# Kernel optimization log

Hardware: AMD Instinct MI355X
Metric: run time of the kernel (lower is better)

Reference implementation:

```python
import jax, jax.numpy as jnp
import numpy as np

GROUP = 128          # GPTQ quantization group size
H = 2048             # hidden_size
I = 1408             # moe_intermediate_size
T = 16384            # routed tokens


def _pack_rows(v):
    # v: [in, out] int4 values -> [in//8, out] int32 (8 nibbles per int32 along input dim)
    v = v.reshape(v.shape[0] // 8, 8, v.shape[1]).astype(jnp.int32)
    sh = (4 * jnp.arange(8, dtype=jnp.int32))[None, :, None]
    return (v << sh).sum(axis=1).astype(jnp.int32)


def _pack_cols(v):
    # v: [groups, out] int4 values -> [groups, out//8] int32
    v = v.reshape(v.shape[0], v.shape[1] // 8, 8).astype(jnp.int32)
    sh = (4 * jnp.arange(8, dtype=jnp.int32))[None, None, :]
    return (v << sh).sum(axis=-1).astype(jnp.int32)


def _unpack_rows(qw):
    # [in//8, out] int32 -> [in, out] int4 values
    sh = 4 * jnp.arange(8, dtype=jnp.int32)
    v = (qw[:, None, :] >> sh[None, :, None]) & 0xF
    return v.reshape(qw.shape[0] * 8, qw.shape[1])


def _unpack_cols(qz):
    # [groups, out//8] int32 -> [groups, out] int4 values
    sh = 4 * jnp.arange(8, dtype=jnp.int32)
    v = (qz[:, :, None] >> sh[None, None, :]) & 0xF
    return v.reshape(qz.shape[0], qz.shape[1] * 8)


def _dequant(qw, qz, sc):
    # GPTQ dequant: W[k, n] = (q[k, n] - (zero[g(k), n] + 1)) * scale[g(k), n]
    w = _unpack_rows(qw).astype(sc.dtype)                      # [in, out]
    z = (_unpack_cols(qz) + 1).astype(sc.dtype)                # [groups, out]
    scale = jnp.repeat(sc, GROUP, axis=0)                      # [in, out]
    zero = jnp.repeat(z, GROUP, axis=0)                        # [in, out]
    return (w - zero) * scale


def setup_inputs() -> dict:
    key = jax.random.key(0)
    ks = jax.random.split(key, 10)
    x = jax.random.normal(ks[0], (T, H), dtype=jnp.float32)

    def make_quant(kq, kz, ksc, n_in, n_out):
        q = jax.random.randint(kq, (n_in, n_out), 0, 16, dtype=jnp.int32)
        z = jax.random.randint(kz, (n_in // GROUP, n_out), 0, 15, dtype=jnp.int32)
        sc = jax.random.uniform(ksc, (n_in // GROUP, n_out), dtype=jnp.float32,
                                minval=1e-3, maxval=2e-2)
        return _pack_rows(q), _pack_cols(z), sc

    qw_g, qz_g, sc_g = make_quant(ks[1], ks[2], ks[3], H, I)
    qw_u, qz_u, sc_u = make_quant(ks[4], ks[5], ks[6], H, I)
    qw_d, qz_d, sc_d = make_quant(ks[7], ks[8], ks[9], I, H)
    return {"x": x,
            "qw_gate": qw_g, "qz_gate": qz_g, "sc_gate": sc_g,
            "qw_up": qw_u, "qz_up": qz_u, "sc_up": sc_u,
            "qw_down": qw_d, "qz_down": qz_d, "sc_down": sc_d}


def reference(x, qw_gate, qz_gate, sc_gate, qw_up, qz_up, sc_up,
              qw_down, qz_down, sc_down):
    Wg = _dequant(qw_gate, qz_gate, sc_gate)   # [H, I]
    Wu = _dequant(qw_up, qz_up, sc_up)         # [H, I]
    Wd = _dequant(qw_down, qz_down, sc_down)   # [I, H]
    # fused_gate_up: silu(x @ Wg) * (x @ Wu)
    h = jax.nn.silu(x @ Wg) * (x @ Wu)         # [T, I]
    return h @ Wd                              # [T, H]
```

## Files before the change

### kernel.cpp

```cpp
#include <hip/hip_runtime.h>

#define T_DIM 16384
#define H_DIM 2048
#define I_DIM 1408
#define NB_DIM (2 * I_DIM)

typedef _Float16 half8 __attribute__((ext_vector_type(8)));
typedef float floatx4 __attribute__((ext_vector_type(4)));

__device__ __forceinline__ void async_cp16(const _Float16* gp, _Float16* lp) {
    __builtin_amdgcn_global_load_lds(
        (const __attribute__((address_space(1))) unsigned int*)gp,
        (__attribute__((address_space(3))) unsigned int*)lp,
        16, 0, 0);
}

__global__ void cvt_fp16_kernel(const float* __restrict__ x, _Float16* __restrict__ xh) {
    int i = (blockIdx.x * 256 + threadIdx.x) * 8;
    const float4* p = (const float4*)(x + i);
    float4 a = p[0];
    float4 b = p[1];
    half8 o = { (_Float16)a.x, (_Float16)a.y, (_Float16)a.z, (_Float16)a.w,
                (_Float16)b.x, (_Float16)b.y, (_Float16)b.z, (_Float16)b.w };
    *(half8*)(xh + i) = o;
}

__global__ void dequant_kernel(const int* __restrict__ qw, const int* __restrict__ qz,
                               const float* __restrict__ sc, _Float16* __restrict__ Wt,
                               int K, int N, int interleave, int off) {
    __shared__ half8 tile[256];
    int t = threadIdx.x;
    int nl = t & 63, kl = t >> 6;
    int n  = blockIdx.x * 64 + nl;
    int kp = blockIdx.y * 4 + kl;
    int q = qw[kp * N + n];
    int g = kp >> 4;
    float scale = sc[g * N + n];
    int zq = (qz[g * (N >> 3) + (n >> 3)] >> (4 * (n & 7))) & 0xF;
    float zf = (float)(zq + 1);
    half8 o;
#pragma unroll
    for (int j = 0; j < 8; ++j)
        o[j] = (_Float16)(((float)((q >> (4 * j)) & 0xF) - zf) * scale);
    tile[nl * 4 + kl] = o;
    __syncthreads();
    int nl2 = t >> 2, kl2 = t & 3;
    int n2 = blockIdx.x * 64 + nl2;
    int np = interleave ? (((n2 >> 5) << 6) + (n2 & 31) + off) : n2;
    *(half8*)(Wt + (size_t)np * K + (size_t)(blockIdx.y * 4 + kl2) * 8) = tile[nl2 * 4 + kl2];
}


__launch_bounds__(256, 3)
__global__ void gemm_gateup(const _Float16* __restrict__ A,
                            const _Float16* __restrict__ B,
                            _Float16* __restrict__ h) {
    __shared__ _Float16 As[128 * 64];
    __shared__ _Float16 Bs[128 * 64];
    const int t = threadIdx.x;
    const int wave = t >> 6, lane = t & 63;
    const int m0 = blockIdx.x * 128;
    const int n0 = blockIdx.y * 128;
    const int wm = wave >> 1, wn = wave & 1;

    const int srow = wave * 8 + (lane >> 3);
    const int schunk = (lane & 7) ^ (lane >> 3);
    const _Float16* ag = A + (size_t)(m0 + srow) * H_DIM + schunk * 8;
    const _Float16* bg = B + (size_t)(n0 + srow) * H_DIM + schunk * 8;
    _Float16* lA = As + wave * 512;
    _Float16* lB = Bs + wave * 512;

    const int q4 = lane >> 4, l15 = lane & 15;
    int aoff[4], boff[4];
#pragma unroll
    for (int i = 0; i < 4; ++i) {
        int rA = wm * 64 + i * 16 + l15;
        aoff[i] = rA * 64 + ((q4 ^ (rA & 7)) * 8);
        int rB = wn * 64 + i * 16 + l15;
        boff[i] = rB * 64 + ((q4 ^ (rB & 7)) * 8);
    }

    floatx4 zero = {0.f, 0.f, 0.f, 0.f};
    floatx4 acc[4][4];
#pragma unroll
    for (int mi = 0; mi < 4; ++mi)
#pragma unroll
        for (int ni = 0; ni < 4; ++ni) acc[mi][ni] = zero;

    for (int kt = 0; kt < H_DIM; kt += 64) {
        __syncthreads();
#pragma unroll
        for (int i = 0; i < 4; ++i) {
            async_cp16(ag + kt + (size_t)i * 32 * H_DIM, lA + i * 2048);
            async_cp16(bg + kt + (size_t)i * 32 * H_DIM, lB + i * 2048);
        }
        __syncthreads();
#pragma unroll
        for (int kk = 0; kk < 2; ++kk) {
            half8 af[4], bf[4];
#pragma unroll
            for (int i = 0; i < 4; ++i) af[i] = *(const half8*)(As + (aoff[i] ^ (kk * 32)));
#pragma unroll
            for (int i = 0; i < 4; ++i) bf[i] = *(const half8*)(Bs + (boff[i] ^ (kk * 32)));
#pragma unroll
            for (int mi = 0; mi < 4; ++mi)
#pragma unroll
                for (int ni = 0; ni < 4; ++ni)
                    acc[mi][ni] = __builtin_amdgcn_mfma_f32_16x16x32_f16(af[mi], bf[ni], acc[mi][ni], 0, 0, 0);
        }
    }

    const int rq = q4 * 4;
#pragma unroll
    for (int mi = 0; mi < 4; ++mi)
#pragma unroll
        for (int nc = 0; nc < 2; ++nc)
#pragma unroll
            for (int r = 0; r < 4; ++r) {
                int row = m0 + wm * 64 + mi * 16 + rq + r;
                int col = blockIdx.y * 64 + wn * 32 + nc * 16 + l15;
                float g = acc[mi][nc][r];
                float u = acc[mi][nc + 2][r];
                float s = (g / (1.0f + __expf(-g))) * u;
                h[(size_t)row * I_DIM + col] = (_Float16)s;
            }
}

__launch_bounds__(256, 3)
__global__ void gemm_down(const _Float16* __restrict__ A,
                          const _Float16* __restrict__ B,
                          float* __restrict__ out) {
    __shared__ _Float16 As[128 * 64];
    __shared__ _Float16 Bs[128 * 64];
    const int t = threadIdx.x;
    const int wave = t >> 6, lane = t & 63;
    const int m0 = blockIdx.x * 128;
    const int n0 = blockIdx.y * 128;
    const int wm = wave >> 1, wn = wave & 1;

    const int srow = wave * 8 + (lane >> 3);
    const int schunk = (lane & 7) ^ (lane >> 3);
    const _Float16* ag = A + (size_t)(m0 + srow) * I_DIM + schunk * 8;
    const _Float16* bg = B + (size_t)(n0 + srow) * I_DIM + schunk * 8;
    _Float16* lA = As + wave * 512;
    _Float16* lB = Bs + wave * 512;

    const int q4 = lane >> 4, l15 = lane & 15;
    int aoff[4], boff[4];
#pragma unroll
    for (int i = 0; i < 4; ++i) {
        int rA = wm * 64 + i * 16 + l15;
        aoff[i] = rA * 64 + ((q4 ^ (rA & 7)) * 8);
        int rB = wn * 64 + i * 16 + l15;
        boff[i] = rB * 64 + ((q4 ^ (rB & 7)) * 8);
    }

    floatx4 zero = {0.f, 0.f, 0.f, 0.f};
    floatx4 acc[4][4];
#pragma unroll
    for (int mi = 0; mi < 4; ++mi)
#pragma unroll
        for (int ni = 0; ni < 4; ++ni) acc[mi][ni] = zero;

    for (int kt = 0; kt < I_DIM; kt += 64) {
        __syncthreads();
#pragma unroll
        for (int i = 0; i < 4; ++i) {
            async_cp16(ag + kt + (size_t)i * 32 * I_DIM, lA + i * 2048);
            async_cp16(bg + kt + (size_t)i * 32 * I_DIM, lB + i * 2048);
        }
        __syncthreads();
#pragma unroll
        for (int kk = 0; kk < 2; ++kk) {
            half8 af[4], bf[4];
#pragma unroll
            for (int i = 0; i < 4; ++i) af[i] = *(const half8*)(As + (aoff[i] ^ (kk * 32)));
#pragma unroll
            for (int i = 0; i < 4; ++i) bf[i] = *(const half8*)(Bs + (boff[i] ^ (kk * 32)));
#pragma unroll
            for (int mi = 0; mi < 4; ++mi)
#pragma unroll
                for (int ni = 0; ni < 4; ++ni)
                    acc[mi][ni] = __builtin_amdgcn_mfma_f32_16x16x32_f16(af[mi], bf[ni], acc[mi][ni], 0, 0, 0);
        }
    }

    const int rq = q4 * 4;
#pragma unroll
    for (int mi = 0; mi < 4; ++mi)
#pragma unroll
        for (int ni = 0; ni < 4; ++ni)
#pragma unroll
            for (int r = 0; r < 4; ++r) {
                int row = m0 + wm * 64 + mi * 16 + rq + r;
                int col = n0 + wn * 64 + ni * 16 + l15;
                out[(size_t)row * H_DIM + col] = acc[ni][mi][r];
            }
}


__launch_bounds__(256, 3)
__global__ void gemm_down_fixed(const _Float16* __restrict__ A,
                                const _Float16* __restrict__ B,
                                float* __restrict__ out) {
    __shared__ _Float16 As[128 * 64];
    __shared__ _Float16 Bs[128 * 64];
    const int t = threadIdx.x;
    const int wave = t >> 6, lane = t & 63;
    const int m0 = blockIdx.x * 128;
    const int n0 = blockIdx.y * 128;
    const int wm = wave >> 1, wn = wave & 1;

    const int srow = wave * 8 + (lane >> 3);
    const int schunk = (lane & 7) ^ (lane >> 3);
    const _Float16* ag = A + (size_t)(m0 + srow) * I_DIM + schunk * 8;
    const _Float16* bg = B + (size_t)(n0 + srow) * I_DIM + schunk * 8;
    _Float16* lA = As + wave * 512;
    _Float16* lB = Bs + wave * 512;

    const int q4 = lane >> 4, l15 = lane & 15;
    int aoff[4], boff[4];
#pragma unroll
    for (int i = 0; i < 4; ++i) {
        int rA = wm * 64 + i * 16 + l15;
        aoff[i] = rA * 64 + ((q4 ^ (rA & 7)) * 8);
        int rB = wn * 64 + i * 16 + l15;
        boff[i] = rB * 64 + ((q4 ^ (rB & 7)) * 8);
    }

    floatx4 zero = {0.f, 0.f, 0.f, 0.f};
    floatx4 acc[4][4];
#pragma unroll
    for (int mi = 0; mi < 4; ++mi)
#pragma unroll
        for (int ni = 0; ni < 4; ++ni) acc[mi][ni] = zero;

    for (int kt = 0; kt < I_DIM; kt += 64) {
        __syncthreads();
#pragma unroll
        for (int i = 0; i < 4; ++i) {
            async_cp16(ag + kt + (size_t)i * 32 * I_DIM, lA + i * 2048);
            async_cp16(bg + kt + (size_t)i * 32 * I_DIM, lB + i * 2048);
        }
        __syncthreads();
#pragma unroll
        for (int kk = 0; kk < 2; ++kk) {
            half8 af[4], bf[4];
#pragma unroll
            for (int i = 0; i < 4; ++i) af[i] = *(const half8*)(As + (aoff[i] ^ (kk * 32)));
#pragma unroll
            for (int i = 0; i < 4; ++i) bf[i] = *(const half8*)(Bs + (boff[i] ^ (kk * 32)));
#pragma unroll
            for (int mi = 0; mi < 4; ++mi)
#pragma unroll
                for (int ni = 0; ni < 4; ++ni)
                    acc[mi][ni] = __builtin_amdgcn_mfma_f32_16x16x32_f16(af[mi], bf[ni], acc[mi][ni], 0, 0, 0);
        }
    }

    const int rq = q4 * 4;
#pragma unroll
    for (int mi = 0; mi < 4; ++mi)
#pragma unroll
        for (int ni = 0; ni < 4; ++ni)
#pragma unroll
            for (int r = 0; r < 4; ++r) {
                int row = m0 + wm * 64 + mi * 16 + rq + r;
                int col = n0 + wn * 64 + ni * 16 + l15;
                out[(size_t)row * H_DIM + col] = acc[mi][ni][r];
            }
}

extern "C" void kernel_launch(void* const* d_in, const int* in_sizes, int n_in,
                              void* d_out, int out_size, void* d_ws, size_t ws_size,
                              hipStream_t stream) {
    const float* x    = (const float*)d_in[0];
    const int* qw_g   = (const int*)d_in[1];
    const int* qz_g   = (const int*)d_in[2];
    const float* sc_g = (const float*)d_in[3];
    const int* qw_u   = (const int*)d_in[4];
    const int* qz_u   = (const int*)d_in[5];
    const float* sc_u = (const float*)d_in[6];
    const int* qw_d   = (const int*)d_in[7];
    const int* qz_d   = (const int*)d_in[8];
    const float* sc_d = (const float*)d_in[9];
    float* out = (float*)d_out;

    char* ws = (char*)d_ws;
    _Float16* xh  = (_Float16*)ws;  ws += (size_t)T_DIM * H_DIM * sizeof(_Float16);
    _Float16* hh  = (_Float16*)ws;  ws += (size_t)T_DIM * I_DIM * sizeof(_Float16);
    _Float16* Bgu = (_Float16*)ws;  ws += (size_t)NB_DIM * H_DIM * sizeof(_Float16);
    _Float16* Wd  = (_Float16*)ws;  ws += (size_t)H_DIM * I_DIM * sizeof(_Float16);

    cvt_fp16_kernel<<<(T_DIM * H_DIM) / 2048, 256, 0, stream>>>(x, xh);
    dequant_kernel<<<dim3(I_DIM / 64, H_DIM / 32), 256, 0, stream>>>(qw_g, qz_g, sc_g, Bgu, H_DIM, I_DIM, 1, 0);
    dequant_kernel<<<dim3(I_DIM / 64, H_DIM / 32), 256, 0, stream>>>(qw_u, qz_u, sc_u, Bgu, H_DIM, I_DIM, 1, 32);
    dequant_kernel<<<dim3(H_DIM / 64, I_DIM / 32), 256, 0, stream>>>(qw_d, qz_d, sc_d, Wd, I_DIM, H_DIM, 0, 0);
    gemm_gateup<<<dim3(T_DIM / 128, NB_DIM / 128), 256, 0, stream>>>(xh, Bgu, hh);
    gemm_down_fixed<<<dim3(T_DIM / 128, H_DIM / 128), 256, 0, stream>>>(hh, Wd, out);
}
```

Before: 518.1 us.

## Switch GEMMs to 32x32x16 MFMA tiles and swap grid axis order

Both GEMM kernels replace the 4x4 grid of 16x16x32 MFMAs per wave with a 2x2 grid of 32x32x16 MFMAs. This halves the LDS fragment loads per k-step and uses the larger, denser matrix instruction. The grid is also transposed so consecutive blocks walk the N dimension for one M tile, which improves L2 reuse of activation rows. The epilogue index mapping is rewritten for the 32x32 accumulator layout, and the duplicate down kernel is removed.

```diff
diff --git a/kernel.cpp b/kernel.cpp
--- a/kernel.cpp
+++ b/kernel.cpp
@@ -6,7 +6,7 @@
 #define NB_DIM (2 * I_DIM)
 
 typedef _Float16 half8 __attribute__((ext_vector_type(8)));
-typedef float floatx4 __attribute__((ext_vector_type(4)));
+typedef float floatx16 __attribute__((ext_vector_type(16)));
 
 __device__ __forceinline__ void async_cp16(const _Float16* gp, _Float16* lp) {
     __builtin_amdgcn_global_load_lds(
@@ -59,8 +59,8 @@
     __shared__ _Float16 Bs[128 * 64];
     const int t = threadIdx.x;
     const int wave = t >> 6, lane = t & 63;
-    const int m0 = blockIdx.x * 128;
-    const int n0 = blockIdx.y * 128;
+    const int n0 = blockIdx.x * 128;
+    const int m0 = blockIdx.y * 128;
     const int wm = wave >> 1, wn = wave & 1;
 
     const int srow = wave * 8 + (lane >> 3);
@@ -70,22 +70,23 @@
     _Float16* lA = As + wave * 512;
     _Float16* lB = Bs + wave * 512;
 
-    const int q4 = lane >> 4, l15 = lane & 15;
-    int aoff[4], boff[4];
-#pragma unroll
-    for (int i = 0; i < 4; ++i) {
-        int rA = wm * 64 + i * 16 + l15;
-        aoff[i] = rA * 64 + ((q4 ^ (rA & 7)) * 8);
-        int rB = wn * 64 + i * 16 + l15;
-        boff[i] = rB * 64 + ((q4 ^ (rB & 7)) * 8);
-    }
-
-    floatx4 zero = {0.f, 0.f, 0.f, 0.f};
-    floatx4 acc[4][4];
-#pragma unroll
-    for (int mi = 0; mi < 4; ++mi)
-#pragma unroll
-        for (int ni = 0; ni < 4; ++ni) acc[mi][ni] = zero;
+    const int l31 = lane & 31, h5 = lane >> 5;
+    int arow64[2], arm[2], brow64[2], brm[2];
+#pragma unroll
+    for (int i = 0; i < 2; ++i) {
+        int rA = wm * 64 + i * 32 + l31;
+        arow64[i] = rA * 64; arm[i] = rA & 7;
+        int rB = wn * 64 + i * 32 + l31;
+        brow64[i] = rB * 64; brm[i] = rB & 7;
+    }
+
+    floatx16 acc[2][2];
+#pragma unroll
+    for (int mi = 0; mi < 2; ++mi)
+#pragma unroll
+        for (int ni = 0; ni < 2; ++ni)
+#pragma unroll
+            for (int r = 0; r < 16; ++r) acc[mi][ni][r] = 0.f;
 
     for (int kt = 0; kt < H_DIM; kt += 64) {
         __syncthreads();
@@ -96,34 +97,32 @@
         }
         __syncthreads();
 #pragma unroll
-        for (int kk = 0; kk < 2; ++kk) {
-            half8 af[4], bf[4];
-#pragma unroll
-            for (int i = 0; i < 4; ++i) af[i] = *(const half8*)(As + (aoff[i] ^ (kk * 32)));
-#pragma unroll
-            for (int i = 0; i < 4; ++i) bf[i] = *(const half8*)(Bs + (boff[i] ^ (kk * 32)));
-#pragma unroll
-            for (int mi = 0; mi < 4; ++mi)
-#pragma unroll
-                for (int ni = 0; ni < 4; ++ni)
-                    acc[mi][ni] = __builtin_amdgcn_mfma_f32_16x16x32_f16(af[mi], bf[ni], acc[mi][ni], 0, 0, 0);
-        }
-    }
-
-    const int rq = q4 * 4;
-#pragma unroll
-    for (int mi = 0; mi < 4; ++mi)
-#pragma unroll
-        for (int nc = 0; nc < 2; ++nc)
-#pragma unroll
-            for (int r = 0; r < 4; ++r) {
-                int row = m0 + wm * 64 + mi * 16 + rq + r;
-                int col = blockIdx.y * 64 + wn * 32 + nc * 16 + l15;
-                float g = acc[mi][nc][r];
-                float u = acc[mi][nc + 2][r];
-                float s = (g / (1.0f + __expf(-g))) * u;
-                h[(size_t)row * I_DIM + col] = (_Float16)s;
-            }
+        for (int kk = 0; kk < 4; ++kk) {
+            const int c = h5 + kk * 2;
+            half8 af[2], bf[2];
+#pragma unroll
+            for (int i = 0; i < 2; ++i) af[i] = *(const half8*)(As + arow64[i] + ((c ^ arm[i]) * 8));
+#pragma unroll
+            for (int i = 0; i < 2; ++i) bf[i] = *(const half8*)(Bs + brow64[i] + ((c ^ brm[i]) * 8));
+#pragma unroll
+            for (int mi = 0; mi < 2; ++mi)
+#pragma unroll
+                for (int ni = 0; ni < 2; ++ni)
+                    acc[mi][ni] = __builtin_amdgcn_mfma_f32_32x32x16_f16(af[mi], bf[ni], acc[mi][ni], 0, 0, 0);
+        }
+    }
+
+    const int hcol = (n0 >> 1) + wn * 32 + l31;
+#pragma unroll
+    for (int mi = 0; mi < 2; ++mi)
+#pragma unroll
+        for (int r = 0; r < 16; ++r) {
+            int row = m0 + wm * 64 + mi * 32 + (r & 3) + 8 * (r >> 2) + 4 * h5;
+            float g = acc[mi][0][r];
+            float u = acc[mi][1][r];
+            float s = (g / (1.0f + __expf(-g))) * u;
+            h[(size_t)row * I_DIM + hcol] = (_Float16)s;
+        }
 }
 
 __launch_bounds__(256, 3)
@@ -134,8 +133,8 @@
     __shared__ _Float16 Bs[128 * 64];
     const int t = threadIdx.x;
     const int wave = t >> 6, lane = t & 63;
-    const int m0 = blockIdx.x * 128;
-    const int n0 = blockIdx.y * 128;
+    const int n0 = blockIdx.x * 128;
+    const int m0 = blockIdx.y * 128;
     const int wm = wave >> 1, wn = wave & 1;
 
     const int srow = wave * 8 + (lane >> 3);
@@ -145,22 +144,23 @@
     _Float16* lA = As + wave * 512;
     _Float16* lB = Bs + wave * 512;
 
-    const int q4 = lane >> 4, l15 = lane & 15;
-    int aoff[4], boff[4];
-#pragma unroll
-    for (int i = 0; i < 4; ++i) {
-        int rA = wm * 64 + i * 16 + l15;
-        aoff[i] = rA * 64 + ((q4 ^ (rA & 7)) * 8);
-        int rB = wn * 64 + i * 16 + l15;
-        boff[i] = rB * 64 + ((q4 ^ (rB & 7)) * 8);
-    }
-
-    floatx4 zero = {0.f, 0.f, 0.f, 0.f};
-    floatx4 acc[4][4];
-#pragma unroll
-    for (int mi = 0; mi < 4; ++mi)
-#pragma unroll
-        for (int ni = 0; ni < 4; ++ni) acc[mi][ni] = zero;
+    const int l31 = lane & 31, h5 = lane >> 5;
+    int arow64[2], arm[2], brow64[2], brm[2];
+#pragma unroll
+    for (int i = 0; i < 2; ++i) {
+        int rA = wm * 64 + i * 32 + l31;
+        arow64[i] = rA * 64; arm[i] = rA & 7;
+        int rB = wn * 64 + i * 32 + l31;
+        brow64[i] = rB * 64; brm[i] = rB & 7;
+    }
+
+    floatx16 acc[2][2];
+#pragma unroll
+    for (int mi = 0; mi < 2; ++mi)
+#pragma unroll
+        for (int ni = 0; ni < 2; ++ni)
+#pragma unroll
+            for (int r = 0; r < 16; ++r) acc[mi][ni][r] = 0.f;
 
     for (int kt = 0; kt < I_DIM; kt += 64) {
         __syncthreads();
@@ -171,102 +171,29 @@
         }
         __syncthreads();
 #pragma unroll
-        for (int kk = 0; kk < 2; ++kk) {
-            half8 af[4], bf[4];
-#pragma unroll
-            for (int i = 0; i < 4; ++i) af[i] = *(const half8*)(As + (aoff[i] ^ (kk * 32)));
-#pragma unroll
-            for (int i = 0; i < 4; ++i) bf[i] = *(const half8*)(Bs + (boff[i] ^ (kk * 32)));
-#pragma unroll
-            for (int mi = 0; mi < 4; ++mi)
-#pragma unroll
-                for (int ni = 0; ni < 4; ++ni)
-                    acc[mi][ni] = __builtin_amdgcn_mfma_f32_16x16x32_f16(af[mi], bf[ni], acc[mi][ni], 0, 0, 0);
-        }
-    }
-
-    const int rq = q4 * 4;
-#pragma unroll
-    for (int mi = 0; mi < 4; ++mi)
-#pragma unroll
-        for (int ni = 0; ni < 4; ++ni)
-#pragma unroll
-            for (int r = 0; r < 4; ++r) {
-                int row = m0 + wm * 64 + mi * 16 + rq + r;
-                int col = n0 + wn * 64 + ni * 16 + l15;
-                out[(size_t)row * H_DIM + col] = acc[ni][mi][r];
-            }
-}
-
-
-__launch_bounds__(256, 3)
-__global__ void gemm_down_fixed(const _Float16* __restrict__ A,
-                                const _Float16* __restrict__ B,
-                                float* __restrict__ out) {
-    __shared__ _Float16 As[128 * 64];
-    __shared__ _Float16 Bs[128 * 64];
-    const int t = threadIdx.x;
-    const int wave = t >> 6, lane = t & 63;
-    const int m0 = blockIdx.x * 128;
-    const int n0 = blockIdx.y * 128;
-    const int wm = wave >> 1, wn = wave & 1;
-
-    const int srow = wave * 8 + (lane >> 3);
-    const int schunk = (lane & 7) ^ (lane >> 3);
-    const _Float16* ag = A + (size_t)(m0 + srow) * I_DIM + schunk * 8;
-    const _Float16* bg = B + (size_t)(n0 + srow) * I_DIM + schunk * 8;
-    _Float16* lA = As + wave * 512;
-    _Float16* lB = Bs + wave * 512;
-
-    const int q4 = lane >> 4, l15 = lane & 15;
-    int aoff[4], boff[4];
-#pragma unroll
-    for (int i = 0; i < 4; ++i) {
-        int rA = wm * 64 + i * 16 + l15;
-        aoff[i] = rA * 64 + ((q4 ^ (rA & 7)) * 8);
-        int rB = wn * 64 + i * 16 + l15;
-        boff[i] = rB * 64 + ((q4 ^ (rB & 7)) * 8);
-    }
-
-    floatx4 zero = {0.f, 0.f, 0.f, 0.f};
-    floatx4 acc[4][4];
-#pragma unroll
-    for (int mi = 0; mi < 4; ++mi)
-#pragma unroll
-        for (int ni = 0; ni < 4; ++ni) acc[mi][ni] = zero;
-
-    for (int kt = 0; kt < I_DIM; kt += 64) {
-        __syncthreads();
-#pragma unroll
-        for (int i = 0; i < 4; ++i) {
-            async_cp16(ag + kt + (size_t)i * 32 * I_DIM, lA + i * 2048);
-            async_cp16(bg + kt + (size_t)i * 32 * I_DIM, lB + i * 2048);
-        }
-        __syncthreads();
-#pragma unroll
-        for (int kk = 0; kk < 2; ++kk) {
-            half8 af[4], bf[4];
-#pragma unroll
-            for (int i = 0; i < 4; ++i) af[i] = *(const half8*)(As + (aoff[i] ^ (kk * 32)));
-#pragma unroll
-            for (int i = 0; i < 4; ++i) bf[i] = *(const half8*)(Bs + (boff[i] ^ (kk * 32)));
-#pragma unroll
-            for (int mi = 0; mi < 4; ++mi)
-#pragma unroll
-                for (int ni = 0; ni < 4; ++ni)
-                    acc[mi][ni] = __builtin_amdgcn_mfma_f32_16x16x32_f16(af[mi], bf[ni], acc[mi][ni], 0, 0, 0);
-        }
-    }
-
-    const int rq = q4 * 4;
-#pragma unroll
-    for (int mi = 0; mi < 4; ++mi)
-#pragma unroll
-        for (int ni = 0; ni < 4; ++ni)
-#pragma unroll
-            for (int r = 0; r < 4; ++r) {
-                int row = m0 + wm * 64 + mi * 16 + rq + r;
-                int col = n0 + wn * 64 + ni * 16 + l15;
+        for (int kk = 0; kk < 4; ++kk) {
+            const int c = h5 + kk * 2;
+            half8 af[2], bf[2];
+#pragma unroll
+            for (int i = 0; i < 2; ++i) af[i] = *(const half8*)(As + arow64[i] + ((c ^ arm[i]) * 8));
+#pragma unroll
+            for (int i = 0; i < 2; ++i) bf[i] = *(const half8*)(Bs + brow64[i] + ((c ^ brm[i]) * 8));
+#pragma unroll
+            for (int mi = 0; mi < 2; ++mi)
+#pragma unroll
+                for (int ni = 0; ni < 2; ++ni)
+                    acc[mi][ni] = __builtin_amdgcn_mfma_f32_32x32x16_f16(af[mi], bf[ni], acc[mi][ni], 0, 0, 0);
+        }
+    }
+
+#pragma unroll
+    for (int mi = 0; mi < 2; ++mi)
+#pragma unroll
+        for (int ni = 0; ni < 2; ++ni)
+#pragma unroll
+            for (int r = 0; r < 16; ++r) {
+                int row = m0 + wm * 64 + mi * 32 + (r & 3) + 8 * (r >> 2) + 4 * h5;
+                int col = n0 + wn * 64 + ni * 32 + l31;
                 out[(size_t)row * H_DIM + col] = acc[mi][ni][r];
             }
 }
@@ -290,12 +217,12 @@
     _Float16* xh  = (_Float16*)ws;  ws += (size_t)T_DIM * H_DIM * sizeof(_Float16);
     _Float16* hh  = (_Float16*)ws;  ws += (size_t)T_DIM * I_DIM * sizeof(_Float16);
     _Float16* Bgu = (_Float16*)ws;  ws += (size_t)NB_DIM * H_DIM * sizeof(_Float16);
-    _Float16* Wd  = (_Float16*)ws;  ws += (size_t)H_DIM * I_DIM * sizeof(_Float16);
+    _Float16* Wd  = (_Float16*)ws;  ws += (size_t)I_DIM * H_DIM * sizeof(_Float16);
 
     cvt_fp16_kernel<<<(T_DIM * H_DIM) / 2048, 256, 0, stream>>>(x, xh);
     dequant_kernel<<<dim3(I_DIM / 64, H_DIM / 32), 256, 0, stream>>>(qw_g, qz_g, sc_g, Bgu, H_DIM, I_DIM, 1, 0);
     dequant_kernel<<<dim3(I_DIM / 64, H_DIM / 32), 256, 0, stream>>>(qw_u, qz_u, sc_u, Bgu, H_DIM, I_DIM, 1, 32);
     dequant_kernel<<<dim3(H_DIM / 64, I_DIM / 32), 256, 0, stream>>>(qw_d, qz_d, sc_d, Wd, I_DIM, H_DIM, 0, 0);
-    gemm_gateup<<<dim3(T_DIM / 128, NB_DIM / 128), 256, 0, stream>>>(xh, Bgu, hh);
-    gemm_down_fixed<<<dim3(T_DIM / 128, H_DIM / 128), 256, 0, stream>>>(hh, Wd, out);
-}
+    gemm_gateup<<<dim3(NB_DIM / 128, T_DIM / 128), 256, 0, stream>>>(xh, Bgu, hh);
+    gemm_down<<<dim3(H_DIM / 128, T_DIM / 128), 256, 0, stream>>>(hh, Wd, out);
+}
```

After: 569.2 us. 1.1x slower.
